# Optimization experiments

Hardware: AMD Instinct MI355X
Metric: run time of the kernel (lower is better)

The kernel has to match this reference:

```python
import jax, jax.numpy as jnp
import numpy as np

N_NODES = 100000
N_EDGES = 500000
HIDDEN = 32
HEADS = 4
PROJ = HIDDEN * HEADS  # 128
LN_EPS = 1e-5


def setup_inputs() -> dict:
    key = jax.random.key(0)
    ks = jax.random.split(key, 12)
    # Xavier-uniform bound for Linear(3, PROJ): sqrt(6/(3+PROJ))
    b_qkv = float(np.sqrt(6.0 / (3 + PROJ)))
    b_out = float(np.sqrt(6.0 / (PROJ + HIDDEN)))
    return {
        "positions": jax.random.normal(ks[0], (N_NODES, 3), dtype=jnp.float32),
        "edge_index": jax.random.randint(ks[1], (2, N_EDGES), 0, N_NODES, dtype=jnp.int64),
        "Wq": jax.random.uniform(ks[2], (3, PROJ), jnp.float32, -b_qkv, b_qkv),
        "bq": jnp.zeros((PROJ,), jnp.float32),
        "Wk": jax.random.uniform(ks[3], (3, PROJ), jnp.float32, -b_qkv, b_qkv),
        "bk": jnp.zeros((PROJ,), jnp.float32),
        "Wv": jax.random.uniform(ks[4], (3, PROJ), jnp.float32, -b_qkv, b_qkv),
        "bv": jnp.zeros((PROJ,), jnp.float32),
        "Wout": jax.random.uniform(ks[5], (PROJ, HIDDEN), jnp.float32, -b_out, b_out),
        "bout": jnp.zeros((HIDDEN,), jnp.float32),
        "gamma": jnp.ones((HIDDEN,), jnp.float32),
        "beta": jnp.zeros((HIDDEN,), jnp.float32),
    }


def reference(positions, edge_index, Wq, bq, Wk, bk, Wv, bv, Wout, bout, gamma, beta):
    row, col = edge_index[0], edge_index[1]
    rel = positions[row] - positions[col]                      # [E, 3]
    E = rel.shape[0]
    q = (rel @ Wq + bq).reshape(E, HEADS, HIDDEN)              # [E, H, D]
    k = (rel @ Wk + bk).reshape(E, HEADS, HIDDEN)
    v = (rel @ Wv + bv).reshape(E, HEADS, HIDDEN)
    # attention score per (edge, head), softmax over heads
    scores = jnp.sum(q * k, axis=-1) / jnp.sqrt(jnp.float32(HIDDEN))  # [E, H]
    attn = jax.nn.softmax(scores, axis=-1)                     # dropout is identity in eval
    wv = (attn[..., None] * v).reshape(E, PROJ)                # [E, H*D]
    # scatter-mean over destination nodes (col), dim_size = N
    seg_sum = jax.ops.segment_sum(wv, col, num_segments=N_NODES)
    counts = jax.ops.segment_sum(jnp.ones((E,), wv.dtype), col, num_segments=N_NODES)
    mean = seg_sum / jnp.maximum(counts, 1.0)[:, None]         # [N, H*D]
    out = mean @ Wout + bout                                   # [N, D]
    mu = jnp.mean(out, axis=-1, keepdims=True)
    var = jnp.var(out, axis=-1, keepdims=True)
    out = (out - mu) / jnp.sqrt(var + LN_EPS) * gamma + beta
    return jax.nn.silu(out)
```

## Files before the change

kernel.cpp:

```cpp
#include <hip/hip_runtime.h>
#include <hip/hip_bf16.h>
#include <hip/hip_fp16.h>

#define LN_EPS 1e-5f

typedef _Float16 f16x2 __attribute__((ext_vector_type(2)));

__device__ __forceinline__ void pk_atomic_add(_Float16* p, float v0, float v1) {
  f16x2 v;
  v.x = (_Float16)v0;
  v.y = (_Float16)v1;
#if __has_builtin(__builtin_amdgcn_flat_atomic_fadd_v2f16)
  __builtin_amdgcn_flat_atomic_fadd_v2f16((f16x2*)p, v);
#else
  unsafeAtomicAdd((__half2*)p, *(__half2*)&v);
#endif
}


__global__ void precompute_kernel(const float* __restrict__ Wq,
                                  const float* __restrict__ bq,
                                  const float* __restrict__ Wk,
                                  const float* __restrict__ bk,
                                  const float* __restrict__ Wv,
                                  const float* __restrict__ bv,
                                  const float* __restrict__ Wout,
                                  const int* __restrict__ ei,
                                  float* __restrict__ flag,
                                  float* __restrict__ coef,
                                  float* __restrict__ T) {
  __shared__ float sM[4][3][32];
  __shared__ float sCv[4][32];
  int t = threadIdx.x;
  const float scale = 0.17677669529663687f;

  if (t == 0) {
    int all_zero = 1;
    for (int i = 0; i < 8; ++i) all_zero &= (ei[2 * i + 1] == 0);
    flag[0] = all_zero ? 1.0f : 0.0f;
  }

  {
    int h = t >> 5, o = t & 31;
    float m0 = 0, m1 = 0, m2 = 0, cv = 0;
    for (int d = 0; d < 32; ++d) {
      int j = h * 32 + d;
      float w = Wout[j * 32 + o];
      m0 += Wv[0 * 128 + j] * w;
      m1 += Wv[1 * 128 + j] * w;
      m2 += Wv[2 * 128 + j] * w;
      cv += bv[j] * w;
    }
    sM[h][0][o] = m0;
    sM[h][1][o] = m1;
    sM[h][2][o] = m2;
    sCv[h][o] = cv;
  }

  if (t < 40) {
    int h = t / 10, j = t % 10;
    float acc = 0;
    for (int d = 0; d < 32; ++d) {
      int idx = h * 32 + d;
      float q0 = Wq[0 * 128 + idx], q1 = Wq[1 * 128 + idx], q2 = Wq[2 * 128 + idx];
      float k0 = Wk[0 * 128 + idx], k1 = Wk[1 * 128 + idx], k2 = Wk[2 * 128 + idx];
      float bqv = bq[idx], bkv = bk[idx];
      float v;
      switch (j) {
        case 0: v = q0 * k0; break;
        case 1: v = q1 * k1; break;
        case 2: v = q2 * k2; break;
        case 3: v = q0 * k1 + q1 * k0; break;
        case 4: v = q0 * k2 + q2 * k0; break;
        case 5: v = q1 * k2 + q2 * k1; break;
        case 6: v = q0 * bkv + k0 * bqv; break;
        case 7: v = q1 * bkv + k1 * bqv; break;
        case 8: v = q2 * bkv + k2 * bqv; break;
        default: v = bqv * bkv; break;
      }
      acc += v;
    }
    coef[h * 10 + j] = acc * scale;
  }

  __syncthreads();

  for (int idx = t; idx < 512; idx += 128) {
    int j = idx >> 5, col = idx & 31;
    float v;
    if (j < 3)        v = sCv[j][col] - sCv[3][col];
    else if (j < 6)   v = sM[3][j - 3][col];
    else if (j < 15)  { int h = (j - 6) / 3, i = (j - 6) % 3; v = sM[h][i][col] - sM[3][i][col]; }
    else              v = sCv[3][col];
    T[idx] = v;
  }
}

__device__ __forceinline__ void sel_comp(int comp, int& pa, int& pr) {
  if (comp < 3)       { pa = comp;           pr = 3; }
  else if (comp < 6)  { pa = 3;              pr = comp - 3; }
  else if (comp < 15) { pa = (comp - 6) / 3; pr = (comp - 6) % 3; }
  else                { pa = 3;              pr = 3; }
}

__global__ void edge_kernel(const float* __restrict__ pos,
                            const int* __restrict__ ei, int E,
                            const float* __restrict__ flag,
                            const float* __restrict__ coef,
                            _Float16* __restrict__ fsums) {
  const int lane = threadIdx.x & 31;
  const int group = (blockIdx.x * blockDim.x + threadIdx.x) >> 5;
  const int base = group * 32;
  if (base >= E) return;

  const int i64 = (flag[0] != 0.0f) ? 1 : 0;
  const int valid_n = min(32, E - base);
  const int e = base + lane;

  int c = 0;
  float rx = 0, ry = 0, rz = 0, a0 = 0, a1 = 0, a2 = 0;
  if (lane < valid_n) {
    int r, cc;
    if (i64) {
      r = ei[2 * (size_t)e];
      cc = ei[2 * ((size_t)E + e)];
    } else {
      r = ei[e];
      cc = ei[E + e];
    }
    c = cc;
    rx = pos[r * 3 + 0] - pos[cc * 3 + 0];
    ry = pos[r * 3 + 1] - pos[cc * 3 + 1];
    rz = pos[r * 3 + 2] - pos[cc * 3 + 2];
    float s[4];
#pragma unroll
    for (int h = 0; h < 4; ++h) {
      const float* cf = coef + h * 10;
      s[h] = cf[9] + rx * cf[6] + ry * cf[7] + rz * cf[8] + rx * rx * cf[0] +
             ry * ry * cf[1] + rz * rz * cf[2] + rx * ry * cf[3] +
             rx * rz * cf[4] + ry * rz * cf[5];
    }
    float mx = fmaxf(fmaxf(s[0], s[1]), fmaxf(s[2], s[3]));
    float e0 = __expf(s[0] - mx), e1 = __expf(s[1] - mx);
    float e2 = __expf(s[2] - mx), e3 = __expf(s[3] - mx);
    float inv = 1.0f / (e0 + e1 + e2 + e3);
    a0 = e0 * inv; a1 = e1 * inv; a2 = e2 * inv;
  }

  const int pair = lane & 7;
  const int sub  = lane >> 3;
  int pa0, pr0, pa1, pr1;
  sel_comp(2 * pair, pa0, pr0);
  sel_comp(2 * pair + 1, pa1, pr1);

  for (int t2 = 0; t2 < valid_n; t2 += 4) {
    const int src = t2 + sub;
    float tx = __shfl(rx, src, 32);
    float ty = __shfl(ry, src, 32);
    float tz = __shfl(rz, src, 32);
    float b0 = __shfl(a0, src, 32);
    float b1 = __shfl(a1, src, 32);
    float b2 = __shfl(a2, src, 32);
    int   ct = __shfl(c,  src, 32);
    float A0 = (pa0 == 0) ? b0 : (pa0 == 1) ? b1 : (pa0 == 2) ? b2 : 1.0f;
    float R0 = (pr0 == 0) ? tx : (pr0 == 1) ? ty : (pr0 == 2) ? tz : 1.0f;
    float A1 = (pa1 == 0) ? b0 : (pa1 == 1) ? b1 : (pa1 == 2) ? b2 : 1.0f;
    float R1 = (pr1 == 0) ? tx : (pr1 == 1) ? ty : (pr1 == 2) ? tz : 1.0f;
    if (src < valid_n)
      pk_atomic_add(fsums + (size_t)ct * 16 + 2 * pair, A0 * R0, A1 * R1);
  }
}

__global__ void node_kernel(const _Float16* __restrict__ fsums,
                            const float* __restrict__ T,
                            const float* __restrict__ bout,
                            const float* __restrict__ gamma,
                            const float* __restrict__ beta,
                            float* __restrict__ out, int N) {
  int tid = blockIdx.x * blockDim.x + threadIdx.x;
  int node = tid >> 5;
  int col = tid & 31;
  if (node >= N) return;

  float myf = (float)fsums[(size_t)node * 16 + (col & 15)];
  float cnt = __shfl(myf, 15, 32);
  float invc = 1.0f / fmaxf(cnt, 1.0f);

  float acc = bout[col];
#pragma unroll
  for (int j = 0; j < 16; ++j) {
    float fj = __shfl(myf, j, 32);
    acc = fmaf(fj * invc, T[j * 32 + col], acc);
  }

  float sx = acc, sx2 = acc * acc;
#pragma unroll
  for (int off = 16; off >= 1; off >>= 1) {
    sx += __shfl_xor(sx, off);
    sx2 += __shfl_xor(sx2, off);
  }
  float mu = sx * (1.0f / 32.0f);
  float var = sx2 * (1.0f / 32.0f) - mu * mu;
  float inv = rsqrtf(var + LN_EPS);
  float y = (acc - mu) * inv * gamma[col] + beta[col];
  float o = y * (1.0f / (1.0f + __expf(-y)));
  out[(size_t)node * 32 + col] = o;
}

extern "C" void kernel_launch(void* const* d_in, const int* in_sizes, int n_in,
                              void* d_out, int out_size, void* d_ws, size_t ws_size,
                              hipStream_t stream) {
  const float* pos  = (const float*)d_in[0];
  const int*   ei   = (const int*)d_in[1];
  const float* Wq   = (const float*)d_in[2];
  const float* bq   = (const float*)d_in[3];
  const float* Wk   = (const float*)d_in[4];
  const float* bk   = (const float*)d_in[5];
  const float* Wv   = (const float*)d_in[6];
  const float* bv   = (const float*)d_in[7];
  const float* Wout = (const float*)d_in[8];
  const float* bout = (const float*)d_in[9];
  const float* gam  = (const float*)d_in[10];
  const float* bet  = (const float*)d_in[11];

  const int N = in_sizes[0] / 3;
  const int E = in_sizes[1] / 2;

  _Float16* fsums = (_Float16*)d_ws;
  float* tail = (float*)((char*)d_ws + (size_t)N * 32);
  float* flag = tail;
  float* coef = flag + 8;
  float* T    = coef + 40;

  hipMemsetAsync(d_ws, 0, (size_t)N * 16 * sizeof(_Float16), stream);

  precompute_kernel<<<1, 128, 0, stream>>>(Wq, bq, Wk, bk, Wv, bv, Wout, ei,
                                           flag, coef, T);

  int edge_blocks = (E + 255) / 256;
  edge_kernel<<<edge_blocks, 256, 0, stream>>>(pos, ei, E, flag, coef, fsums);

  int node_blocks = (int)(((size_t)N * 32 + 255) / 256);
  node_kernel<<<node_blocks, 256, 0, stream>>>(fsums, T, bout, gam, bet,
                                               (float*)d_out, N);

  (void)n_in; (void)out_size; (void)ws_size;
}
```

Measured before the change: 142.7 us.

## Fuse precompute into edge kernel and vectorize node feature loads

Removes the single-block precompute launch. Each edge block now recomputes the 40 attention coefficients into shared memory, and block 0 also writes the T projection table. The node kernel loads its 16 fp16 sums as two 8-wide vectors instead of using shuffles, and the int64 edge index is read as int2. This trades one launch and a serial dependency for redundant per-block coefficient math, which puts a small loop of weight loads before every block's edge work.

```diff
diff --git a/kernel.cpp b/kernel.cpp
--- a/kernel.cpp
+++ b/kernel.cpp
@@ -1,10 +1,10 @@
 #include <hip/hip_runtime.h>
-#include <hip/hip_bf16.h>
 #include <hip/hip_fp16.h>
 
 #define LN_EPS 1e-5f
 
 typedef _Float16 f16x2 __attribute__((ext_vector_type(2)));
+typedef _Float16 f16x8 __attribute__((ext_vector_type(8)));
 
 __device__ __forceinline__ void pk_atomic_add(_Float16* p, float v0, float v1) {
   f16x2 v;
@@ -18,52 +18,41 @@
 }
 
 
-__global__ void precompute_kernel(const float* __restrict__ Wq,
-                                  const float* __restrict__ bq,
-                                  const float* __restrict__ Wk,
-                                  const float* __restrict__ bk,
-                                  const float* __restrict__ Wv,
-                                  const float* __restrict__ bv,
-                                  const float* __restrict__ Wout,
-                                  const int* __restrict__ ei,
-                                  float* __restrict__ flag,
-                                  float* __restrict__ coef,
-                                  float* __restrict__ T) {
+__device__ __forceinline__ void sel_comp(int comp, int& pa, int& pr) {
+  if (comp < 3)       { pa = comp;           pr = 3; }
+  else if (comp < 6)  { pa = 3;              pr = comp - 3; }
+  else if (comp < 15) { pa = (comp - 6) / 3; pr = (comp - 6) % 3; }
+  else                { pa = 3;              pr = 3; }
+}
+
+__global__ __launch_bounds__(256) void edge_kernel(
+    const float* __restrict__ pos, const int* __restrict__ ei, int E,
+    const float* __restrict__ Wq, const float* __restrict__ bq,
+    const float* __restrict__ Wk, const float* __restrict__ bk,
+    const float* __restrict__ Wv, const float* __restrict__ bv,
+    const float* __restrict__ Wout, float* __restrict__ T,
+    _Float16* __restrict__ fsums) {
+  __shared__ float scoef[40];
+  __shared__ int sflag;
   __shared__ float sM[4][3][32];
   __shared__ float sCv[4][32];
-  int t = threadIdx.x;
+  const int t = threadIdx.x;
   const float scale = 0.17677669529663687f;
 
   if (t == 0) {
     int all_zero = 1;
+#pragma unroll
     for (int i = 0; i < 8; ++i) all_zero &= (ei[2 * i + 1] == 0);
-    flag[0] = all_zero ? 1.0f : 0.0f;
-  }
-
-  {
-    int h = t >> 5, o = t & 31;
-    float m0 = 0, m1 = 0, m2 = 0, cv = 0;
+    sflag = all_zero;
+  }
+
+  if (t < 40) {
+    const int h = t / 10, j = t % 10;
+    float acc = 0.f;
     for (int d = 0; d < 32; ++d) {
-      int j = h * 32 + d;
-      float w = Wout[j * 32 + o];
-      m0 += Wv[0 * 128 + j] * w;
-      m1 += Wv[1 * 128 + j] * w;
-      m2 += Wv[2 * 128 + j] * w;
-      cv += bv[j] * w;
-    }
-    sM[h][0][o] = m0;
-    sM[h][1][o] = m1;
-    sM[h][2][o] = m2;
-    sCv[h][o] = cv;
-  }
-
-  if (t < 40) {
-    int h = t / 10, j = t % 10;
-    float acc = 0;
-    for (int d = 0; d < 32; ++d) {
-      int idx = h * 32 + d;
-      float q0 = Wq[0 * 128 + idx], q1 = Wq[1 * 128 + idx], q2 = Wq[2 * 128 + idx];
-      float k0 = Wk[0 * 128 + idx], k1 = Wk[1 * 128 + idx], k2 = Wk[2 * 128 + idx];
+      const int idx = h * 32 + d;
+      float q0 = Wq[idx], q1 = Wq[128 + idx], q2 = Wq[256 + idx];
+      float k0 = Wk[idx], k1 = Wk[128 + idx], k2 = Wk[256 + idx];
       float bqv = bq[idx], bkv = bk[idx];
       float v;
       switch (j) {
@@ -80,40 +69,46 @@
       }
       acc += v;
     }
-    coef[h * 10 + j] = acc * scale;
+    scoef[t] = acc * scale;
+  }
+
+  if (blockIdx.x == 0 && t < 128) {
+    const int h = t >> 5, o = t & 31;
+    float m0 = 0, m1 = 0, m2 = 0, cv = 0;
+    for (int d = 0; d < 32; ++d) {
+      const int j = h * 32 + d;
+      const float w = Wout[j * 32 + o];
+      m0 += Wv[j] * w;
+      m1 += Wv[128 + j] * w;
+      m2 += Wv[256 + j] * w;
+      cv += bv[j] * w;
+    }
+    sM[h][0][o] = m0;
+    sM[h][1][o] = m1;
+    sM[h][2][o] = m2;
+    sCv[h][o] = cv;
   }
 
   __syncthreads();
 
-  for (int idx = t; idx < 512; idx += 128) {
-    int j = idx >> 5, col = idx & 31;
-    float v;
-    if (j < 3)        v = sCv[j][col] - sCv[3][col];
-    else if (j < 6)   v = sM[3][j - 3][col];
-    else if (j < 15)  { int h = (j - 6) / 3, i = (j - 6) % 3; v = sM[h][i][col] - sM[3][i][col]; }
-    else              v = sCv[3][col];
-    T[idx] = v;
-  }
-}
-
-__device__ __forceinline__ void sel_comp(int comp, int& pa, int& pr) {
-  if (comp < 3)       { pa = comp;           pr = 3; }
-  else if (comp < 6)  { pa = 3;              pr = comp - 3; }
-  else if (comp < 15) { pa = (comp - 6) / 3; pr = (comp - 6) % 3; }
-  else                { pa = 3;              pr = 3; }
-}
-
-__global__ void edge_kernel(const float* __restrict__ pos,
-                            const int* __restrict__ ei, int E,
-                            const float* __restrict__ flag,
-                            const float* __restrict__ coef,
-                            _Float16* __restrict__ fsums) {
-  const int lane = threadIdx.x & 31;
-  const int group = (blockIdx.x * blockDim.x + threadIdx.x) >> 5;
+  if (blockIdx.x == 0) {
+    for (int idx = t; idx < 512; idx += 256) {
+      const int j = idx >> 5, col = idx & 31;
+      float v;
+      if (j < 3)        v = sCv[j][col] - sCv[3][col];
+      else if (j < 6)   v = sM[3][j - 3][col];
+      else if (j < 15)  { const int h = (j - 6) / 3, i = (j - 6) % 3; v = sM[h][i][col] - sM[3][i][col]; }
+      else              v = sCv[3][col];
+      T[idx] = v;
+    }
+  }
+
+  const int lane = t & 31;
+  const int group = (blockIdx.x * blockDim.x + t) >> 5;
   const int base = group * 32;
   if (base >= E) return;
 
-  const int i64 = (flag[0] != 0.0f) ? 1 : 0;
+  const int i64 = sflag;
   const int valid_n = min(32, E - base);
   const int e = base + lane;
 
@@ -122,11 +117,13 @@
   if (lane < valid_n) {
     int r, cc;
     if (i64) {
-      r = ei[2 * (size_t)e];
-      cc = ei[2 * ((size_t)E + e)];
+      const int2 pr = ((const int2*)ei)[(size_t)e];
+      const int2 pc = ((const int2*)ei)[(size_t)E + (size_t)e];
+      r = pr.x;
+      cc = pc.x;
     } else {
       r = ei[e];
-      cc = ei[E + e];
+      cc = ei[(size_t)E + e];
     }
     c = cc;
     rx = pos[r * 3 + 0] - pos[cc * 3 + 0];
@@ -135,7 +132,7 @@
     float s[4];
 #pragma unroll
     for (int h = 0; h < 4; ++h) {
-      const float* cf = coef + h * 10;
+      const float* cf = scoef + h * 10;
       s[h] = cf[9] + rx * cf[6] + ry * cf[7] + rz * cf[8] + rx * rx * cf[0] +
              ry * ry * cf[1] + rz * rz * cf[2] + rx * ry * cf[3] +
              rx * rz * cf[4] + ry * rz * cf[5];
@@ -171,27 +168,30 @@
   }
 }
 
-__global__ void node_kernel(const _Float16* __restrict__ fsums,
-                            const float* __restrict__ T,
-                            const float* __restrict__ bout,
-                            const float* __restrict__ gamma,
-                            const float* __restrict__ beta,
-                            float* __restrict__ out, int N) {
-  int tid = blockIdx.x * blockDim.x + threadIdx.x;
-  int node = tid >> 5;
-  int col = tid & 31;
+__global__ __launch_bounds__(256) void node_kernel(
+    const _Float16* __restrict__ fsums, const float* __restrict__ T,
+    const float* __restrict__ bout, const float* __restrict__ gamma,
+    const float* __restrict__ beta, float* __restrict__ out, int N) {
+  const int tid = blockIdx.x * blockDim.x + threadIdx.x;
+  const int node = tid >> 5;
+  const int col = tid & 31;
   if (node >= N) return;
 
-  float myf = (float)fsums[(size_t)node * 16 + (col & 15)];
-  float cnt = __shfl(myf, 15, 32);
-  float invc = 1.0f / fmaxf(cnt, 1.0f);
-
-  float acc = bout[col];
-#pragma unroll
-  for (int j = 0; j < 16; ++j) {
-    float fj = __shfl(myf, j, 32);
-    acc = fmaf(fj * invc, T[j * 32 + col], acc);
-  }
+  const f16x8* fp = (const f16x8*)(fsums + (size_t)node * 16);
+  const f16x8 va = fp[0];
+  const f16x8 vb = fp[1];
+  float f[16];
+#pragma unroll
+  for (int j = 0; j < 8; ++j) {
+    f[j] = (float)va[j];
+    f[8 + j] = (float)vb[j];
+  }
+  const float invc = 1.0f / fmaxf(f[15], 1.0f);
+
+  float acc = 0.f;
+#pragma unroll
+  for (int j = 0; j < 16; ++j) acc = fmaf(f[j], T[j * 32 + col], acc);
+  acc = fmaf(acc, invc, bout[col]);
 
   float sx = acc, sx2 = acc * acc;
 #pragma unroll
@@ -199,11 +199,11 @@
     sx += __shfl_xor(sx, off);
     sx2 += __shfl_xor(sx2, off);
   }
-  float mu = sx * (1.0f / 32.0f);
-  float var = sx2 * (1.0f / 32.0f) - mu * mu;
-  float inv = rsqrtf(var + LN_EPS);
-  float y = (acc - mu) * inv * gamma[col] + beta[col];
-  float o = y * (1.0f / (1.0f + __expf(-y)));
+  const float mu = sx * (1.0f / 32.0f);
+  const float var = sx2 * (1.0f / 32.0f) - mu * mu;
+  const float inv = rsqrtf(var + LN_EPS);
+  const float y = (acc - mu) * inv * gamma[col] + beta[col];
+  const float o = y * (1.0f / (1.0f + __expf(-y)));
   out[(size_t)node * 32 + col] = o;
 }
 
@@ -227,20 +227,15 @@
   const int E = in_sizes[1] / 2;
 
   _Float16* fsums = (_Float16*)d_ws;
-  float* tail = (float*)((char*)d_ws + (size_t)N * 32);
-  float* flag = tail;
-  float* coef = flag + 8;
-  float* T    = coef + 40;
-
-  hipMemsetAsync(d_ws, 0, (size_t)N * 16 * sizeof(_Float16), stream);
-
-  precompute_kernel<<<1, 128, 0, stream>>>(Wq, bq, Wk, bk, Wv, bv, Wout, ei,
-                                           flag, coef, T);
-
-  int edge_blocks = (E + 255) / 256;
-  edge_kernel<<<edge_blocks, 256, 0, stream>>>(pos, ei, E, flag, coef, fsums);
-
-  int node_blocks = (int)(((size_t)N * 32 + 255) / 256);
+  float* T = (float*)((char*)d_ws + (size_t)N * 32);
+
+  hipMemsetAsync(d_ws, 0, (size_t)N * 32, stream);
+
+  const int edge_blocks = (E + 255) / 256;
+  edge_kernel<<<edge_blocks, 256, 0, stream>>>(pos, ei, E, Wq, bq, Wk, bk, Wv,
+                                               bv, Wout, T, fsums);
+
+  const int node_blocks = (int)(((size_t)N * 32 + 255) / 256);
   node_kernel<<<node_blocks, 256, 0, stream>>>(fsums, T, bout, gam, bet,
                                                (float*)d_out, N);
 
```

New measurement: 157.2 us. 1.1x slower.
